# Performance work log

Measured on AMD Instinct MI355X. Metric: run time of the kernel, lower is better.

## Reference

```python
import jax, jax.numpy as jnp
import numpy as np

H = 256  # hidden size (hardcoded in module)
F_IN = 10  # input features (hardcoded via x.view(..., 10))


def _lstm_cell(x, h, c, w_ih, w_hh, b_ih, b_hh):
    # PyTorch gate order: i, f, g, o. gates: [B, 4H]
    gates = x @ w_ih.T + h @ w_hh.T + b_ih + b_hh
    i, f, g, o = jnp.split(gates, 4, axis=-1)
    c_new = jax.nn.sigmoid(f) * c + jax.nn.sigmoid(i) * jnp.tanh(g)
    h_new = jax.nn.sigmoid(o) * jnp.tanh(c_new)
    return h_new, c_new


def setup_inputs() -> dict:
    key = jax.random.key(0)
    ks = jax.random.split(key, 13)
    B, T = 512, 1024
    s = 0.05
    return {
        "x": jax.random.normal(ks[0], (B, T, F_IN), dtype=jnp.float32),
        "w_ih0": jax.random.normal(ks[1], (4 * H, F_IN), dtype=jnp.float32) * s,
        "w_hh0": jax.random.normal(ks[2], (4 * H, H), dtype=jnp.float32) * s,
        "b_ih0": jax.random.normal(ks[3], (4 * H,), dtype=jnp.float32) * s,
        "b_hh0": jax.random.normal(ks[4], (4 * H,), dtype=jnp.float32) * s,
        "w_ih1": jax.random.normal(ks[5], (4 * H, H), dtype=jnp.float32) * s,
        "w_hh1": jax.random.normal(ks[6], (4 * H, H), dtype=jnp.float32) * s,
        "b_ih1": jax.random.normal(ks[7], (4 * H,), dtype=jnp.float32) * s,
        "b_hh1": jax.random.normal(ks[8], (4 * H,), dtype=jnp.float32) * s,
        "adv_w1": jax.random.normal(ks[9], (H, H), dtype=jnp.float32) * s,
        "adv_b1": jax.random.normal(ks[10], (H,), dtype=jnp.float32) * s,
        "adv_w2": jax.random.normal(ks[11], (1, H), dtype=jnp.float32) * s,
        "adv_b2": jax.random.normal(ks[12], (1,), dtype=jnp.float32) * s,
    }


def reference(x, w_ih0, w_hh0, b_ih0, b_hh0, w_ih1, w_hh1, b_ih1, b_hh1,
              adv_w1, adv_b1, adv_w2, adv_b2):
    B, T, _ = x.shape
    h0 = jnp.zeros((B, H), dtype=x.dtype)

    def step(carry, x_t):
        h1, c1, h2, c2 = carry
        h1, c1 = _lstm_cell(x_t, h1, c1, w_ih0, w_hh0, b_ih0, b_hh0)
        h2, c2 = _lstm_cell(h1, h2, c2, w_ih1, w_hh1, b_ih1, b_hh1)
        return (h1, c1, h2, c2), h2

    xs = jnp.swapaxes(x, 0, 1)  # [T, B, F_IN]
    _, hs = jax.lax.scan(step, (h0, h0, h0, h0), xs)  # hs: [T, B, H]

    # advantage MLP head applied per-timestep
    hidden = jax.nn.relu(jnp.einsum('tbh,oh->tbo', hs, adv_w1) + adv_b1)
    scores = jnp.einsum('tbh,oh->tbo', hidden, adv_w2) + adv_b2  # [T, B, 1]

    # Faithful to torch.cat(outputs).view(B, -1): flatten TIME-major, then
    # reinterpret as [B, T] (mixes batch and time when B != T).
    flat = scores.reshape(-1)            # time-major flat buffer [T*B]
    mixed = flat.reshape(B, T)
    advantage = jax.nn.softmax(mixed, axis=1)
    return advantage.reshape(-1)
```

## Files before the change

### kernel.cpp

```cpp
#include <hip/hip_runtime.h>
#include <cstdint>
#include <cstddef>

#define Tn 1024
#define Bn 512
#define Hn 256

#define H1S 264
#define H2S 264
#define WHS 264
#define GWS 20

#define H1_OFF   0
#define H1B_OFF  (H1_OFF + 16*H1S*2)
#define H2_OFF   (H1B_OFF + 16*H1S*2)
#define XB_OFF   (H2_OFF + 16*H2S*2)
#define WH_OFF   (XB_OFF + 2*16*16*2)
#define GW_OFF   (WH_OFF + 16*WHS*2)
#define B1_OFF   (GW_OFF + 4*16*GWS*4)
#define B2_OFF   (B1_OFF + 64*4)
#define BH_OFF   (B2_OFF + 64*4)
#define W2H_OFF  (BH_OFF + 16*4)
#define SYNC_OFF (W2H_OFF + 16*4)
#define LDS_TOTAL 79872

#define SCORES_OFF 0
#define H1G_OFF  (2*1024*1024)
#define H2G_OFF  (3*1024*1024)
#define FLAG_OFF (4*1024*1024)
#define WS_USED  (4*1024*1024 + 8192)

#define POLL_GUARD (1 << 22)

typedef _Float16 v4h __attribute__((ext_vector_type(4)));
typedef float    v4f __attribute__((ext_vector_type(4)));
typedef unsigned int u32x4 __attribute__((ext_vector_type(4)));
typedef unsigned long long u64;

__device__ inline float sigm(float x){ return 1.0f/(1.0f + __expf(-x)); }
__device__ inline float tanh_f(float x){ return 1.0f - 2.0f/(1.0f + __expf(2.0f*x)); }

__device__ inline v4h cvt4(float4 a){
    v4h f; f[0]=(_Float16)a.x; f[1]=(_Float16)a.y; f[2]=(_Float16)a.z; f[3]=(_Float16)a.w;
    return f;
}

__device__ inline bool poll32(const int* tags, int tgt){
    int idx = threadIdx.x & 31;
    int guard = 0;
    while (true){
        int t = __hip_atomic_load(&tags[idx], __ATOMIC_RELAXED, __HIP_MEMORY_SCOPE_AGENT);
        if (__ballot(t < tgt) == 0ull) return true;
        if (++guard > POLL_GUARD) return false;
        __builtin_amdgcn_s_sleep(1);
    }
}

__device__ __forceinline__ bool ebar2(volatile int* c, int target, volatile int* deadp){
    asm volatile("s_waitcnt lgkmcnt(0)" ::: "memory");
    if ((threadIdx.x & 63) == 0) atomicAdd((int*)c, 1);
    int guard = 0;
    while (*c < target){
        if (*deadp) return false;
        if (++guard > POLL_GUARD){ *deadp = 1; return false; }
    }
    asm volatile("" ::: "memory");
    return true;
}

#define LADDR(oo) ( (size_t)(((oo)>>9)*528 + ((oo)&511)) )
__device__ __forceinline__ void stage_tile8w(const char* gbase, char* lbase, int l){
    u32x4 q0,q1,q2,q3,q4,q5,q6,q7;
    const char* p = gbase + l*16;
    asm volatile("global_load_dwordx4 %0, %1, off sc0 sc1" : "=v"(q0) : "v"(p));
    asm volatile("global_load_dwordx4 %0, %1, off sc0 sc1" : "=v"(q1) : "v"(p+1024));
    asm volatile("global_load_dwordx4 %0, %1, off sc0 sc1" : "=v"(q2) : "v"(p+2048));
    asm volatile("global_load_dwordx4 %0, %1, off sc0 sc1" : "=v"(q3) : "v"(p+3072));
    asm volatile("global_load_dwordx4 %0, %1, off sc0 sc1" : "=v"(q4) : "v"(p+4096));
    asm volatile("global_load_dwordx4 %0, %1, off sc0 sc1" : "=v"(q5) : "v"(p+5120));
    asm volatile("global_load_dwordx4 %0, %1, off sc0 sc1" : "=v"(q6) : "v"(p+6144));
    asm volatile("global_load_dwordx4 %0, %1, off sc0 sc1" : "=v"(q7) : "v"(p+7168));
    asm volatile("s_waitcnt vmcnt(0)"
                 : "+v"(q0), "+v"(q1), "+v"(q2), "+v"(q3),
                   "+v"(q4), "+v"(q5), "+v"(q6), "+v"(q7) :: "memory");
    const int o = l*16;
    *(u32x4*)(lbase + LADDR(o))        = q0;
    *(u32x4*)(lbase + LADDR(o + 1024)) = q1;
    *(u32x4*)(lbase + LADDR(o + 2048)) = q2;
    *(u32x4*)(lbase + LADDR(o + 3072)) = q3;
    *(u32x4*)(lbase + LADDR(o + 4096)) = q4;
    *(u32x4*)(lbase + LADDR(o + 5120)) = q5;
    *(u32x4*)(lbase + LADDR(o + 6144)) = q6;
    *(u32x4*)(lbase + LADDR(o + 7168)) = q7;
}

__device__ __forceinline__ void lstm_ew_publish(v4f acc, float* gw, const float* bs,
                                                int n, float& c, _Float16* dst,
                                                int ln15, int ln4)
{
    #pragma unroll
    for (int r = 0; r < 4; ++r) gw[(ln4*4 + r)*GWS + ln15] = acc[r];
    asm volatile("s_waitcnt lgkmcnt(0)" ::: "memory");
    v4f g4 = *(const v4f*)(gw + ln15*GWS + ln4*4);
    asm volatile("s_waitcnt lgkmcnt(0)" ::: "memory");
    v4f bb = *(const v4f*)(bs + n*16 + ln4*4);
    float gi = sigm(g4.x + bb.x), gf = sigm(g4.y + bb.y);
    float gg = tanh_f(g4.z + bb.z), go = sigm(g4.w + bb.w);
    c = gf*c + gi*gg;
    float hn = go * tanh_f(c);
    union { _Float16 h; unsigned short u; } cvt; cvt.h = (_Float16)hn;
    unsigned v32 = cvt.u;
    unsigned p16 = (unsigned)__shfl_xor((int)v32, 16, 64);
    unsigned lo32 = v32 | (p16 << 16);
    unsigned hi32 = (unsigned)__shfl_xor((int)lo32, 32, 64);
    if (ln4 == 0){
        u64 pk = (u64)lo32 | ((u64)hi32 << 32);
        __hip_atomic_store((u64*)dst, pk, __ATOMIC_RELAXED, __HIP_MEMORY_SCOPE_AGENT);
    }
}

__global__ __launch_bounds__(256)
void lstm_pipe(const float* __restrict__ x,
               const float* __restrict__ w_ih0, const float* __restrict__ w_hh0,
               const float* __restrict__ b_ih0, const float* __restrict__ b_hh0,
               const float* __restrict__ w_ih1, const float* __restrict__ w_hh1,
               const float* __restrict__ b_ih1, const float* __restrict__ b_hh1,
               const float* __restrict__ adv_w1, const float* __restrict__ adv_b1,
               const float* __restrict__ adv_w2,
               float* __restrict__ scores, _Float16* __restrict__ h1g,
               _Float16* __restrict__ h2g, int* __restrict__ flags)
{
    extern __shared__ char smem[];
    _Float16* H1l = (_Float16*)(smem + H1_OFF);
    _Float16* H1B = (_Float16*)(smem + H1B_OFF);
    _Float16* H2l = (_Float16*)(smem + H2_OFF);
    _Float16* XBp = (_Float16*)(smem + XB_OFF);
    _Float16* WHl = (_Float16*)(smem + WH_OFF);
    float* gatesc = (float*)(smem + GW_OFF);
    float* b1s    = (float*)(smem + B1_OFF);
    float* b2s    = (float*)(smem + B2_OFF);
    float* bhs    = (float*)(smem + BH_OFF);
    float* w2hs   = (float*)(smem + W2H_OFF);
    volatile int* eb0   = (volatile int*)(smem + SYNC_OFF);
    volatile int* eb1   = (volatile int*)(smem + SYNC_OFF + 4);
    volatile int* e1p   = (volatile int*)(smem + SYNC_OFF + 8);
    volatile int* deadp = (volatile int*)(smem + SYNC_OFF + 12);

    const int tid  = threadIdx.x;
    const int lane = tid & 63;
    const int wv   = tid >> 6;
    const int ln15 = lane & 15;
    const int ln4  = lane >> 4;
    const int rt = blockIdx.x >> 4;
    const int us = blockIdx.x & 15;
    const int r0 = rt * 16;
    const int u0 = us * 16;
    const int eng = wv >> 1;
    const int wq  = wv & 1;
    const int n0  = wq * 2;

    int* tags1 = flags;
    int* tags2 = flags + 1024;

    if (tid == 0){ *eb0 = 0; *eb1 = 0; *e1p = 0; *deadp = 0; }

    const int N0i = n0*16 + ln15;
    const int R0 = (N0i & 3)*256 + u0 + (N0i >> 2);
    const int N1i = N0i + 16;
    const int R1 = (N1i & 3)*256 + u0 + (N1i >> 2);
    v4h W[64];
    if (eng == 0){
        #pragma unroll
        for (int t = 0; t < 2; ++t){
            const int R = t ? R1 : R0;
            v4h f;
            #pragma unroll
            for (int j = 0; j < 4; ++j){
                int c = ln4*4 + j;
                f[j] = (_Float16)((c < 10) ? w_ih0[R*10 + c] : 0.f);
            }
            W[t] = f;
        }
        #pragma unroll
        for (int k = 0; k < 16; ++k){
            float4 a0 = *(const float4*)(w_hh0 + (size_t)R0*256 + k*16 + ln4*4);
            float4 a1 = *(const float4*)(w_hh0 + (size_t)R1*256 + k*16 + ln4*4);
            W[2+k]  = cvt4(a0);
            W[18+k] = cvt4(a1);
        }
    } else {
        #pragma unroll
        for (int k = 0; k < 16; ++k){
            float4 a0 = *(const float4*)(w_ih1 + (size_t)R0*256 + k*16 + ln4*4);
            float4 a1 = *(const float4*)(w_ih1 + (size_t)R1*256 + k*16 + ln4*4);
            float4 b0 = *(const float4*)(w_hh1 + (size_t)R0*256 + k*16 + ln4*4);
            float4 b1 = *(const float4*)(w_hh1 + (size_t)R1*256 + k*16 + ln4*4);
            W[k]    = cvt4(a0);
            W[16+k] = cvt4(a1);
            W[32+k] = cvt4(b0);
            W[48+k] = cvt4(b1);
        }
    }

    for (int idx = tid; idx < 16*WHS; idx += 256){
        int n = idx / WHS, c = idx - n*WHS;
        float v = (c < 256) ? adv_w1[(u0+n)*256 + c] : 0.f;
        WHl[idx] = (_Float16)v;
    }
    if (tid < 64){
        int R = (tid & 3)*256 + u0 + (tid >> 2);
        b1s[tid] = b_ih0[R] + b_hh0[R];
        b2s[tid] = b_ih1[R] + b_hh1[R];
    }
    if (tid < 16){
        bhs[tid]  = adv_b1[u0 + tid];
        w2hs[tid] = adv_w2[u0 + tid];
    }
    for (int idx = tid; idx < 512; idx += 256) XBp[idx] = (_Float16)0.f;
    __syncthreads();
    if (tid < 16){
        const float* xp = x + ((size_t)(r0 + tid)*Tn + 0)*10;
        #pragma unroll
        for (int i = 0; i < 10; ++i) XBp[tid*16 + i] = (_Float16)xp[i];
    }
    __syncthreads();

    float ca = 0.f, cb = 0.f;
    float* gw = gatesc + wv*(16*GWS);

    if (eng == 0){
        int bgen = 0;
        for (int tau = 0; tau < Tn; ++tau){
            float xr[10];
            if (wq == 1 && lane < 16 && tau + 1 < Tn){
                const float* xp = x + ((size_t)(r0 + lane)*Tn + (tau+1))*10;
                #pragma unroll
                for (int i = 0; i < 10; ++i) xr[i] = xp[i];
            }
            if (tau >= 3){
                int guard = 0;
                while (*e1p < tau - 2){
                    if (*deadp) return;
                    if (++guard > POLL_GUARD){ *deadp = 1; return; }
                }
            }
            if (wq == 0){
                if (tau >= 1){
                    if (!poll32(tags1 + rt*32, tau)){ *deadp = 1; return; }
                }
                asm volatile("" ::: "memory");
                const int slot = (tau + 3) & 3;
                stage_tile8w((const char*)(h1g + (size_t)slot*(Bn*Hn) + (size_t)r0*Hn),
                             (char*)H1l, lane);
            } else {
                if (lane < 16 && tau + 1 < Tn){
                    _Float16* xd = XBp + ((tau+1) & 1)*256 + lane*16;
                    #pragma unroll
                    for (int i = 0; i < 10; ++i) xd[i] = (_Float16)xr[i];
                }
            }
            ++bgen; if (!ebar2(eb0, 2*bgen, deadp)) return;

            v4f acc0 = {0.f,0.f,0.f,0.f}, acc1 = {0.f,0.f,0.f,0.f};
            {
                v4h a = *(const v4h*)(XBp + (tau & 1)*256 + ln15*16 + ln4*4);
                acc0 = __builtin_amdgcn_mfma_f32_16x16x16f16(a, W[0], acc0, 0,0,0);
                acc1 = __builtin_amdgcn_mfma_f32_16x16x16f16(a, W[1], acc1, 0,0,0);
            }
            const _Float16* Ap = H1l + ln15*H1S + ln4*4;
            #pragma unroll
            for (int k = 0; k < 16; ++k){
                v4h a = *(const v4h*)(Ap + k*16);
                acc0 = __builtin_amdgcn_mfma_f32_16x16x16f16(a, W[2+k],  acc0, 0,0,0);
                acc1 = __builtin_amdgcn_mfma_f32_16x16x16f16(a, W[18+k], acc1, 0,0,0);
            }
            _Float16* d0 = h1g + (size_t)(tau & 3)*(Bn*Hn)
                         + (size_t)(r0 + ln15)*Hn + u0 + n0*4;
            lstm_ew_publish(acc0, gw, b1s, n0,   ca, d0,     ln15, ln4);
            lstm_ew_publish(acc1, gw, b1s, n0+1, cb, d0 + 4, ln15, ln4);
            asm volatile("s_waitcnt vmcnt(0)" ::: "memory");
            if (lane == 0)
                __hip_atomic_store(&tags1[rt*32 + us*2 + wq], tau + 1,
                                   __ATOMIC_RELAXED, __HIP_MEMORY_SCOPE_AGENT);
            ++bgen; if (!ebar2(eb0, 2*bgen, deadp)) return;
        }
    } else {
        int bgen = 0;
        for (int tau = 1; tau <= Tn + 1; ++tau){
            if (wq == 0){
                if (tau <= Tn){
                    if (!poll32(tags1 + rt*32, tau)){ *deadp = 1; return; }
                    asm volatile("" ::: "memory");
                    const int slot = (tau + 3) & 3;
                    stage_tile8w((const char*)(h1g + (size_t)slot*(Bn*Hn) + (size_t)r0*Hn),
                                 (char*)H1B, lane);
                }
            } else {
                if (tau >= 2){
                    if (!poll32(tags2 + rt*32, tau - 1)){ *deadp = 1; return; }
                }
                asm volatile("" ::: "memory");
                const int slot = (tau + 2) & 3;
                stage_tile8w((const char*)(h2g + (size_t)slot*(Bn*Hn) + (size_t)r0*Hn),
                             (char*)H2l, lane);
            }
            ++bgen; if (!ebar2(eb1, 2*bgen, deadp)) return;
            if (wq == 0 && lane == 0) *e1p = tau;

            if (tau <= Tn){
                v4f acc0 = {0.f,0.f,0.f,0.f}, acc1 = {0.f,0.f,0.f,0.f};
                const _Float16* Ap1 = H1B + ln15*H1S + ln4*4;
                const _Float16* Ap2 = H2l + ln15*H2S + ln4*4;
                #pragma unroll
                for (int k = 0; k < 16; ++k){
                    v4h a = *(const v4h*)(Ap1 + k*16);
                    acc0 = __builtin_amdgcn_mfma_f32_16x16x16f16(a, W[k],    acc0, 0,0,0);
                    acc1 = __builtin_amdgcn_mfma_f32_16x16x16f16(a, W[16+k], acc1, 0,0,0);
                }
                #pragma unroll
                for (int k = 0; k < 16; ++k){
                    v4h a = *(const v4h*)(Ap2 + k*16);
                    acc0 = __builtin_amdgcn_mfma_f32_16x16x16f16(a, W[32+k], acc0, 0,0,0);
                    acc1 = __builtin_amdgcn_mfma_f32_16x16x16f16(a, W[48+k], acc1, 0,0,0);
                }
                _Float16* d0 = h2g + (size_t)((tau + 3) & 3)*(Bn*Hn)
                             + (size_t)(r0 + ln15)*Hn + u0 + n0*4;
                lstm_ew_publish(acc0, gw, b2s, n0,   ca, d0,     ln15, ln4);
                lstm_ew_publish(acc1, gw, b2s, n0+1, cb, d0 + 4, ln15, ln4);
                asm volatile("s_waitcnt vmcnt(0)" ::: "memory");
                if (lane == 0)
                    __hip_atomic_store(&tags2[rt*32 + us*2 + wq], tau,
                                       __ATOMIC_RELAXED, __HIP_MEMORY_SCOPE_AGENT);
            }
            if (wq == 0 && tau >= 2){
                v4f acc = {0.f,0.f,0.f,0.f};
                const _Float16* Ap = H2l + ln15*H2S + ln4*4;
                const _Float16* Bp = WHl + ln15*WHS + ln4*4;
                #pragma unroll
                for (int k = 0; k < 16; ++k)
                    acc = __builtin_amdgcn_mfma_f32_16x16x16f16(*(const v4h*)(Ap + k*16),
                                                                *(const v4h*)(Bp + k*16), acc, 0, 0, 0);
                float bh = bhs[ln15], w2 = w2hs[ln15];
                float t0 = fmaxf(acc[0] + bh, 0.f) * w2;
                float t1 = fmaxf(acc[1] + bh, 0.f) * w2;
                float t2 = fmaxf(acc[2] + bh, 0.f) * w2;
                float t3 = fmaxf(acc[3] + bh, 0.f) * w2;
                #pragma unroll
                for (int mk = 1; mk <= 8; mk <<= 1){
                    t0 += __shfl_xor(t0, mk, 64);
                    t1 += __shfl_xor(t1, mk, 64);
                    t2 += __shfl_xor(t2, mk, 64);
                    t3 += __shfl_xor(t3, mk, 64);
                }
                if (ln15 == 0){
                    float* sp = scores + (size_t)(tau - 2)*Bn + r0 + ln4*4;
                    atomicAdd(sp + 0, t0);
                    atomicAdd(sp + 1, t1);
                    atomicAdd(sp + 2, t2);
                    atomicAdd(sp + 3, t3);
                }
            }
            ++bgen; if (!ebar2(eb1, 2*bgen, deadp)) return;
        }
    }
}

__global__ __launch_bounds__(256)
void softmax_adv(const float* __restrict__ scores, float* __restrict__ out)
{
    const int b = blockIdx.x, tid = threadIdx.x;
    const int lane = tid & 63, wv = tid >> 6;
    __shared__ float red[4];
    const float4* sp = (const float4*)(scores + (size_t)b*1024);
    float4 v = sp[tid];
    float m = fmaxf(fmaxf(v.x, v.y), fmaxf(v.z, v.w));
    #pragma unroll
    for (int o = 32; o > 0; o >>= 1) m = fmaxf(m, __shfl_xor(m, o, 64));
    if (lane == 0) red[wv] = m;
    __syncthreads();
    m = fmaxf(fmaxf(red[0], red[1]), fmaxf(red[2], red[3]));
    __syncthreads();
    float e0 = __expf(v.x - m), e1 = __expf(v.y - m);
    float e2 = __expf(v.z - m), e3 = __expf(v.w - m);
    float s = e0 + e1 + e2 + e3;
    #pragma unroll
    for (int o = 32; o > 0; o >>= 1) s += __shfl_xor(s, o, 64);
    if (lane == 0) red[wv] = s;
    __syncthreads();
    s = red[0] + red[1] + red[2] + red[3];
    float inv = 1.0f / s;
    float4 o4; o4.x = e0*inv; o4.y = e1*inv; o4.z = e2*inv; o4.w = e3*inv;
    ((float4*)(out + (size_t)b*1024))[tid] = o4;
}

extern "C" void kernel_launch(void* const* d_in, const int* in_sizes, int n_in,
                              void* d_out, int out_size, void* d_ws, size_t ws_size,
                              hipStream_t stream)
{
    (void)in_sizes; (void)n_in; (void)out_size; (void)ws_size;
    const float* x      = (const float*)d_in[0];
    const float* w_ih0  = (const float*)d_in[1];
    const float* w_hh0  = (const float*)d_in[2];
    const float* b_ih0  = (const float*)d_in[3];
    const float* b_hh0  = (const float*)d_in[4];
    const float* w_ih1  = (const float*)d_in[5];
    const float* w_hh1  = (const float*)d_in[6];
    const float* b_ih1  = (const float*)d_in[7];
    const float* b_hh1  = (const float*)d_in[8];
    const float* adv_w1 = (const float*)d_in[9];
    const float* adv_b1 = (const float*)d_in[10];
    const float* adv_w2 = (const float*)d_in[11];

    float*    scores = (float*)((char*)d_ws + SCORES_OFF);
    _Float16* h1g    = (_Float16*)((char*)d_ws + H1G_OFF);
    _Float16* h2g    = (_Float16*)((char*)d_ws + H2G_OFF);
    int*      flags  = (int*)((char*)d_ws + FLAG_OFF);

    hipMemsetAsync(d_ws, 0, WS_USED, stream);
    hipFuncSetAttribute((const void*)lstm_pipe,
                        hipFuncAttributeMaxDynamicSharedMemorySize, LDS_TOTAL);

    hipLaunchKernelGGL(lstm_pipe, dim3(512), dim3(256), LDS_TOTAL, stream,
                       x, w_ih0, w_hh0, b_ih0, b_hh0, w_ih1, w_hh1, b_ih1, b_hh1,
                       adv_w1, adv_b1, adv_w2, scores, h1g, h2g, flags);
    hipLaunchKernelGGL(softmax_adv, dim3(512), dim3(256), 0, stream,
                       scores, (float*)d_out);
}
```

Before: 4.691 ms.

## Decouple layer-0 waves with private H1 staging and global-flag backpressure

Each layer-0 wave now stages its own private copy of the h1 tile and loads its x slice straight from global memory into registers. This removes the shared x double buffer and the intra-block barriers between the two layer-0 waves. The LDS-based e1p throttle from layer 1 is replaced by polling the global layer-2 tags before publishing, which still protects the 4-slot h1 ring. The aim is to shorten the per-step critical path of the layer-0 recurrence, at the cost of duplicate staging loads and an extra poll on the global flags.

```diff
diff --git a/kernel.cpp b/kernel.cpp
--- a/kernel.cpp
+++ b/kernel.cpp
@@ -11,17 +11,16 @@
 #define WHS 264
 #define GWS 20
 
-#define H1_OFF   0
-#define H1B_OFF  (H1_OFF + 16*H1S*2)
-#define H2_OFF   (H1B_OFF + 16*H1S*2)
-#define XB_OFF   (H2_OFF + 16*H2S*2)
-#define WH_OFF   (XB_OFF + 2*16*16*2)
-#define GW_OFF   (WH_OFF + 16*WHS*2)
-#define B1_OFF   (GW_OFF + 4*16*GWS*4)
-#define B2_OFF   (B1_OFF + 64*4)
-#define BH_OFF   (B2_OFF + 64*4)
-#define W2H_OFF  (BH_OFF + 16*4)
-#define SYNC_OFF (W2H_OFF + 16*4)
+#define H1P_OFF  0
+#define H1B_OFF  16896
+#define H2_OFF   25344
+#define WH_OFF   33792
+#define GW_OFF   42240
+#define B1_OFF   47360
+#define B2_OFF   47616
+#define BH_OFF   47872
+#define W2H_OFF  47936
+#define SYNC_OFF 48000
 #define LDS_TOTAL 79872
 
 #define SCORES_OFF 0
@@ -131,20 +130,16 @@
                _Float16* __restrict__ h2g, int* __restrict__ flags)
 {
     extern __shared__ char smem[];
-    _Float16* H1l = (_Float16*)(smem + H1_OFF);
     _Float16* H1B = (_Float16*)(smem + H1B_OFF);
     _Float16* H2l = (_Float16*)(smem + H2_OFF);
-    _Float16* XBp = (_Float16*)(smem + XB_OFF);
     _Float16* WHl = (_Float16*)(smem + WH_OFF);
     float* gatesc = (float*)(smem + GW_OFF);
     float* b1s    = (float*)(smem + B1_OFF);
     float* b2s    = (float*)(smem + B2_OFF);
     float* bhs    = (float*)(smem + BH_OFF);
     float* w2hs   = (float*)(smem + W2H_OFF);
-    volatile int* eb0   = (volatile int*)(smem + SYNC_OFF);
-    volatile int* eb1   = (volatile int*)(smem + SYNC_OFF + 4);
-    volatile int* e1p   = (volatile int*)(smem + SYNC_OFF + 8);
-    volatile int* deadp = (volatile int*)(smem + SYNC_OFF + 12);
+    volatile int* eb1   = (volatile int*)(smem + SYNC_OFF);
+    volatile int* deadp = (volatile int*)(smem + SYNC_OFF + 4);
 
     const int tid  = threadIdx.x;
     const int lane = tid & 63;
@@ -162,7 +157,7 @@
     int* tags1 = flags;
     int* tags2 = flags + 1024;
 
-    if (tid == 0){ *eb0 = 0; *eb1 = 0; *e1p = 0; *deadp = 0; }
+    if (tid == 0){ *eb1 = 0; *deadp = 0; }
 
     const int N0i = n0*16 + ln15;
     const int R0 = (N0i & 3)*256 + u0 + (N0i >> 2);
@@ -216,63 +211,48 @@
         bhs[tid]  = adv_b1[u0 + tid];
         w2hs[tid] = adv_w2[u0 + tid];
     }
-    for (int idx = tid; idx < 512; idx += 256) XBp[idx] = (_Float16)0.f;
-    __syncthreads();
-    if (tid < 16){
-        const float* xp = x + ((size_t)(r0 + tid)*Tn + 0)*10;
-        #pragma unroll
-        for (int i = 0; i < 10; ++i) XBp[tid*16 + i] = (_Float16)xp[i];
-    }
     __syncthreads();
 
     float ca = 0.f, cb = 0.f;
     float* gw = gatesc + wv*(16*GWS);
 
     if (eng == 0){
-        int bgen = 0;
+        _Float16* H1P = (_Float16*)(smem + H1P_OFF + wq*8448);
         for (int tau = 0; tau < Tn; ++tau){
-            float xr[10];
-            if (wq == 1 && lane < 16 && tau + 1 < Tn){
-                const float* xp = x + ((size_t)(r0 + lane)*Tn + (tau+1))*10;
-                #pragma unroll
-                for (int i = 0; i < 10; ++i) xr[i] = xp[i];
-            }
-            if (tau >= 3){
-                int guard = 0;
-                while (*e1p < tau - 2){
-                    if (*deadp) return;
-                    if (++guard > POLL_GUARD){ *deadp = 1; return; }
-                }
-            }
-            if (wq == 0){
-                if (tau >= 1){
-                    if (!poll32(tags1 + rt*32, tau)){ *deadp = 1; return; }
-                }
-                asm volatile("" ::: "memory");
-                const int slot = (tau + 3) & 3;
-                stage_tile8w((const char*)(h1g + (size_t)slot*(Bn*Hn) + (size_t)r0*Hn),
-                             (char*)H1l, lane);
-            } else {
-                if (lane < 16 && tau + 1 < Tn){
-                    _Float16* xd = XBp + ((tau+1) & 1)*256 + lane*16;
-                    #pragma unroll
-                    for (int i = 0; i < 10; ++i) xd[i] = (_Float16)xr[i];
-                }
-            }
-            ++bgen; if (!ebar2(eb0, 2*bgen, deadp)) return;
+            float xv0 = 0.f, xv1 = 0.f, xv2 = 0.f, xv3 = 0.f;
+            {
+                const float* xrow = x + ((size_t)(r0 + ln15)*Tn + tau)*10;
+                if (ln4 < 2){
+                    float2 a = *(const float2*)(xrow + ln4*4);
+                    float2 b = *(const float2*)(xrow + ln4*4 + 2);
+                    xv0 = a.x; xv1 = a.y; xv2 = b.x; xv3 = b.y;
+                } else if (ln4 == 2){
+                    float2 a = *(const float2*)(xrow + 8);
+                    xv0 = a.x; xv1 = a.y;
+                }
+            }
+            if (tau >= 1){
+                if (!poll32(tags1 + rt*32, tau)){ *deadp = 1; return; }
+            }
+            asm volatile("" ::: "memory");
+            const int slot = (tau + 3) & 3;
+            stage_tile8w((const char*)(h1g + (size_t)slot*(Bn*Hn) + (size_t)r0*Hn),
+                         (char*)H1P, lane);
+            v4h xa; xa[0] = (_Float16)xv0; xa[1] = (_Float16)xv1;
+                    xa[2] = (_Float16)xv2; xa[3] = (_Float16)xv3;
 
             v4f acc0 = {0.f,0.f,0.f,0.f}, acc1 = {0.f,0.f,0.f,0.f};
-            {
-                v4h a = *(const v4h*)(XBp + (tau & 1)*256 + ln15*16 + ln4*4);
-                acc0 = __builtin_amdgcn_mfma_f32_16x16x16f16(a, W[0], acc0, 0,0,0);
-                acc1 = __builtin_amdgcn_mfma_f32_16x16x16f16(a, W[1], acc1, 0,0,0);
-            }
-            const _Float16* Ap = H1l + ln15*H1S + ln4*4;
+            acc0 = __builtin_amdgcn_mfma_f32_16x16x16f16(xa, W[0], acc0, 0,0,0);
+            acc1 = __builtin_amdgcn_mfma_f32_16x16x16f16(xa, W[1], acc1, 0,0,0);
+            const _Float16* Ap = H1P + ln15*H1S + ln4*4;
             #pragma unroll
             for (int k = 0; k < 16; ++k){
                 v4h a = *(const v4h*)(Ap + k*16);
                 acc0 = __builtin_amdgcn_mfma_f32_16x16x16f16(a, W[2+k],  acc0, 0,0,0);
                 acc1 = __builtin_amdgcn_mfma_f32_16x16x16f16(a, W[18+k], acc1, 0,0,0);
+            }
+            if (tau >= 2){
+                if (!poll32(tags2 + rt*32, tau - 2)){ *deadp = 1; return; }
             }
             _Float16* d0 = h1g + (size_t)(tau & 3)*(Bn*Hn)
                          + (size_t)(r0 + ln15)*Hn + u0 + n0*4;
@@ -282,7 +262,6 @@
             if (lane == 0)
                 __hip_atomic_store(&tags1[rt*32 + us*2 + wq], tau + 1,
                                    __ATOMIC_RELAXED, __HIP_MEMORY_SCOPE_AGENT);
-            ++bgen; if (!ebar2(eb0, 2*bgen, deadp)) return;
         }
     } else {
         int bgen = 0;
@@ -291,8 +270,8 @@
                 if (tau <= Tn){
                     if (!poll32(tags1 + rt*32, tau)){ *deadp = 1; return; }
                     asm volatile("" ::: "memory");
-                    const int slot = (tau + 3) & 3;
-                    stage_tile8w((const char*)(h1g + (size_t)slot*(Bn*Hn) + (size_t)r0*Hn),
+                    stage_tile8w((const char*)(h1g + (size_t)((tau+3)&3)*(Bn*Hn)
+                                               + (size_t)r0*Hn),
                                  (char*)H1B, lane);
                 }
             } else {
@@ -300,12 +279,11 @@
                     if (!poll32(tags2 + rt*32, tau - 1)){ *deadp = 1; return; }
                 }
                 asm volatile("" ::: "memory");
-                const int slot = (tau + 2) & 3;
-                stage_tile8w((const char*)(h2g + (size_t)slot*(Bn*Hn) + (size_t)r0*Hn),
+                stage_tile8w((const char*)(h2g + (size_t)((tau+2)&3)*(Bn*Hn)
+                                           + (size_t)r0*Hn),
                              (char*)H2l, lane);
             }
             ++bgen; if (!ebar2(eb1, 2*bgen, deadp)) return;
-            if (wq == 0 && lane == 0) *e1p = tau;
 
             if (tau <= Tn){
                 v4f acc0 = {0.f,0.f,0.f,0.f}, acc1 = {0.f,0.f,0.f,0.f};
```

Result: faster. 4.143 ms (-11.7%).
